# Optimization experiments

Hardware: AMD Instinct MI355X
Metric: run time of the kernel (lower is better)

Reference implementation:

```python
import jax, jax.numpy as jnp
import numpy as np

N, E, D_IN, D, H = 50000, 600000, 128, 128, 128
NEG_SLOPE = 0.2  # PyG GATConv default


def setup_inputs() -> dict:
    key = jax.random.key(0)
    ks = jax.random.split(key, 10)
    s = 1.0 / np.sqrt(D)
    return {
        "x": jax.random.normal(ks[0], (N, D_IN), jnp.float32),
        "edge_index": jax.random.randint(ks[1], (2, E), 0, N, jnp.int64),
        "h": jax.random.normal(ks[2], (1, N, H), jnp.float32),
        "c": jax.random.normal(ks[3], (1, N, H), jnp.float32),
        "W": jax.random.normal(ks[4], (D_IN, D), jnp.float32) * s,
        "att_src": jax.random.normal(ks[5], (D,), jnp.float32) * s,
        "att_dst": jax.random.normal(ks[6], (D,), jnp.float32) * s,
        "bias_gat": jnp.zeros((D,), jnp.float32),
        "W_ih": jax.random.normal(ks[7], (4 * H, D), jnp.float32) * s,
        "W_hh": jax.random.normal(ks[8], (4 * H, H), jnp.float32) * s,
    }


def _gat_conv(x, edge_index, W, att_src, att_dst, bias_gat):
    n = x.shape[0]
    xs = x @ W  # [N, D]
    # add self loops (PyG default add_self_loops=True)
    loop = jnp.arange(n, dtype=edge_index.dtype)
    src = jnp.concatenate([edge_index[0], loop])
    dst = jnp.concatenate([edge_index[1], loop])
    a_src = xs @ att_src  # [N]
    a_dst = xs @ att_dst  # [N]
    e = a_src[src] + a_dst[dst]  # [E+N]
    e = jnp.where(e >= 0, e, NEG_SLOPE * e)  # leaky_relu
    # segment softmax over edges grouped by destination node
    e_max = jax.ops.segment_max(e, dst, num_segments=n)
    e_exp = jnp.exp(e - e_max[dst])
    e_sum = jax.ops.segment_sum(e_exp, dst, num_segments=n)
    alpha = e_exp / (e_sum[dst] + 1e-16)  # [E+N]
    out = jax.ops.segment_sum(alpha[:, None] * xs[src], dst, num_segments=n)
    return out + bias_gat


def _lstm_step(x, h0, c0, W_ih, W_hh):
    # torch LSTM gate order: i, f, g, o; bias=False
    gates = x @ W_ih.T + h0 @ W_hh.T  # [N, 4H]
    i, f, g, o = jnp.split(gates, 4, axis=-1)
    i, f, o = jax.nn.sigmoid(i), jax.nn.sigmoid(f), jax.nn.sigmoid(o)
    g = jnp.tanh(g)
    c1 = f * c0 + i * g
    h1 = o * jnp.tanh(c1)
    return h1, c1


def reference(x, edge_index, h, c, W, att_src, att_dst, bias_gat, W_ih, W_hh):
    xb = jnp.tanh(_gat_conv(x, edge_index, W, att_src, att_dst, bias_gat))  # [N, D]
    h1, c1 = _lstm_step(xb, h[0], c[0], W_ih, W_hh)
    # LSTM output for seq_len=1 equals the new hidden state
    return xb * 0 + h1, h1[None], c1[None]
```

## Files before the change

kernel.cpp:

```cpp
#include <hip/hip_runtime.h>
#include <hip/hip_bf16.h>
#include <math.h>

#define NEG 0.2f

typedef float f32x4 __attribute__((ext_vector_type(4)));
typedef short bf16x8 __attribute__((ext_vector_type(8)));

__device__ __forceinline__ float fsig(float x){ return 1.0f/(1.0f+__expf(-x)); }
__device__ __forceinline__ float ftanh(float x){ float e = __expf(2.0f*x); return 1.0f - 2.0f/(e+1.0f); }
__device__ __forceinline__ unsigned short f2bf(float v){
    __hip_bfloat16 b = __float2bfloat16(v);
    return *(unsigned short*)&b;
}
__device__ __forceinline__ bf16x8 pack8(float4 u, float4 v){
    bf16x8 r;
    r[0]=(short)f2bf(u.x); r[1]=(short)f2bf(u.y); r[2]=(short)f2bf(u.z); r[3]=(short)f2bf(u.w);
    r[4]=(short)f2bf(v.x); r[5]=(short)f2bf(v.y); r[6]=(short)f2bf(v.z); r[7]=(short)f2bf(v.w);
    return r;
}

__global__ void k_probe(const int* __restrict__ ei, int* __restrict__ flag){
    if(threadIdx.x==0){
        int nz=0;
        for(int i=0;i<64;i++) nz |= ei[2*i+1];
        *flag = (nz==0) ? 1 : 0;
    }
}

__global__ __launch_bounds__(256) void k_wpackx(const float* __restrict__ W,
                                                unsigned short* __restrict__ WPX){
    int f = blockIdx.x*256 + threadIdx.x;
    int l = f&63, ct = (f>>6)&7, ks = f>>9;
    int k0 = ks*32 + (l>>4)*8;
    int col = ct*16 + (l&15);
    #pragma unroll
    for(int j=0;j<8;j++) WPX[(size_t)f*8+j] = f2bf(W[(size_t)(k0+j)*128 + col]);
}

__global__ __launch_bounds__(256) void k_wtpack2(const float* __restrict__ W_ih,
                                                 const float* __restrict__ W_hh,
                                                 unsigned short* __restrict__ WP2){
    int f = blockIdx.x*256 + threadIdx.x;
    int l = f&63, ct = (f>>6)&3, ks = (f>>8)&7, g = f>>11;
    int k0 = ks*32 + (l>>4)*8;
    int col = ct*128 + g*16 + (l&15);
    #pragma unroll
    for(int j=0;j<8;j++){
        int k = k0+j;
        float w = (k<128) ? W_ih[(size_t)col*128+k] : W_hh[(size_t)col*128+(k-128)];
        WP2[(size_t)f*8+j] = f2bf(w);
    }
}

__global__ __launch_bounds__(256,2) void k_gemm_xs3(const float* __restrict__ x,
                                                    const unsigned short* __restrict__ WPX,
                                                    const float* __restrict__ att_s,
                                                    const float* __restrict__ att_d,
                                                    unsigned short* __restrict__ xsb,
                                                    float* __restrict__ a_src,
                                                    float* __restrict__ a_dst,
                                                    int n, int ntiles, int nwaves){
    const int w = threadIdx.x>>6, l = threadIdx.x&63;
    const int wid = blockIdx.x*4 + w;
    bf16x8 B[32];
    #pragma unroll
    for(int f=0;f<32;f++) B[f] = *(const bf16x8*)(WPX + (size_t)(f*64 + l)*8);
    float asv[8], adv[8];
    #pragma unroll
    for(int ct=0;ct<8;ct++){
        asv[ct] = att_s[ct*16 + (l&15)];
        adv[ct] = att_d[ct*16 + (l&15)];
    }
    for(int rt = wid; rt < ntiles; rt += nwaves){
        int arow = rt*16 + (l&15); if(arow>=n) arow = n-1;
        const float* xr = x + (size_t)arow*128 + (l>>4)*8;
        bf16x8 A[4];
        #pragma unroll
        for(int ks=0;ks<4;ks++){
            float4 u = *(const float4*)(xr + ks*32);
            float4 v = *(const float4*)(xr + ks*32 + 4);
            A[ks] = pack8(u,v);
        }
        f32x4 acc[8];
        #pragma unroll
        for(int ct=0;ct<8;ct++) acc[ct] = (f32x4){0.f,0.f,0.f,0.f};
        #pragma unroll
        for(int ks=0;ks<4;ks++){
            #pragma unroll
            for(int ct=0;ct<8;ct++)
                acc[ct] = __builtin_amdgcn_mfma_f32_16x16x32_bf16(A[ks], B[ks*8+ct], acc[ct], 0,0,0);
        }
        #pragma unroll
        for(int reg=0;reg<4;reg++){
            int row = rt*16 + (l>>4)*4 + reg;
            float ps=0.f, pd=0.f;
            #pragma unroll
            for(int ct=0;ct<8;ct++){ ps += acc[ct][reg]*asv[ct]; pd += acc[ct][reg]*adv[ct]; }
            ps += __shfl_xor(ps,1); pd += __shfl_xor(pd,1);
            ps += __shfl_xor(ps,2); pd += __shfl_xor(pd,2);
            ps += __shfl_xor(ps,4); pd += __shfl_xor(pd,4);
            ps += __shfl_xor(ps,8); pd += __shfl_xor(pd,8);
            if((l&15)==0 && row<n){ a_src[row]=ps; a_dst[row]=pd; }
            if(row<n){
                #pragma unroll
                for(int ct=0;ct<8;ct++)
                    xsb[(size_t)row*128 + ct*16 + (l&15)] = f2bf(acc[ct][reg]);
            }
        }
    }
}

__global__ __launch_bounds__(256) void k_hist(const int* __restrict__ ei,
                                              const int* __restrict__ flag,
                                              int* __restrict__ deg, int E, int EN){
    int e = blockIdx.x*256 + threadIdx.x;
    if(e>=EN) return;
    int dst = (e>=E) ? (e-E) : (*flag ? ei[2*(E+e)] : ei[E+e]);
    atomicAdd(&deg[dst], 1);
}

__global__ __launch_bounds__(256) void k_scan1(const int* __restrict__ deg,
                                               int* __restrict__ bsum, int n){
    __shared__ int ws[4];
    int b = blockIdx.x, t = threadIdx.x;
    int i = b*512 + t*2;
    int s = 0;
    if(i<n)   s += deg[i];
    if(i+1<n) s += deg[i+1];
    for(int off=32;off;off>>=1) s += __shfl_xor(s,off);
    if((t&63)==0) ws[t>>6]=s;
    __syncthreads();
    if(t==0) bsum[b]=ws[0]+ws[1]+ws[2]+ws[3];
}

__global__ void k_scan2(int* __restrict__ bsum, int* __restrict__ rowptr,
                        int nb, int n, int EN){
    int t = threadIdx.x;
    int v0 = (t<nb)    ? bsum[t]    : 0;
    int v1 = (64+t<nb) ? bsum[64+t] : 0;
    int x = v0;
    for(int d=1; d<64; d<<=1){ int y=__shfl_up(x,d); if(t>=d) x+=y; }
    int tot0 = __shfl(x,63);
    int x1 = v1;
    for(int d=1; d<64; d<<=1){ int y=__shfl_up(x1,d); if(t>=d) x1+=y; }
    if(t<nb)    bsum[t]    = x - v0;
    if(64+t<nb) bsum[64+t] = tot0 + x1 - v1;
    if(t==0) rowptr[n]=EN;
}

__global__ __launch_bounds__(256) void k_scan3(const int* __restrict__ deg,
                                               const int* __restrict__ bsum,
                                               int* __restrict__ rowptr,
                                               int* __restrict__ cursor, int n){
    __shared__ int wsum[4];
    int b = blockIdx.x, t = threadIdx.x;
    int i = b*512 + t*2;
    int d0 = (i<n)?deg[i]:0, d1 = (i+1<n)?deg[i+1]:0;
    int s = d0+d1;
    int x = s;
    int lane = t&63, wv = t>>6;
    for(int dd=1; dd<64; dd<<=1){ int y=__shfl_up(x,dd); if(lane>=dd) x+=y; }
    if(lane==63) wsum[wv]=x;
    __syncthreads();
    int woff=0;
    for(int w=0;w<wv;w++) woff += wsum[w];
    int ex = bsum[b] + woff + x - s;
    if(i<n)   { rowptr[i]  =ex;    cursor[i]  =ex;    }
    if(i+1<n) { rowptr[i+1]=ex+d0; cursor[i+1]=ex+d0; }
}

__global__ __launch_bounds__(256) void k_fill(const int* __restrict__ ei,
                                              const int* __restrict__ flag,
                                              int* __restrict__ cursor,
                                              int* __restrict__ csr_src, int E, int EN){
    int e = blockIdx.x*256 + threadIdx.x;
    if(e>=EN) return;
    int src,dst;
    if(e>=E){ src=dst=e-E; }
    else if(*flag){ src = ei[2*e]; dst = ei[2*(E+e)]; }
    else         { src = ei[e];   dst = ei[E+e]; }
    int pos = atomicAdd(&cursor[dst], 1);
    csr_src[pos] = src;
}

__global__ __launch_bounds__(256) void k_agg3(const int* __restrict__ rowptr,
                                              const int* __restrict__ csr_src,
                                              const float* __restrict__ a_src,
                                              const float* __restrict__ a_dst,
                                              const unsigned int* __restrict__ xsb32,
                                              const float* __restrict__ bg,
                                              const float* __restrict__ h0,
                                              unsigned short* __restrict__ xh, int n){
    const int wv = threadIdx.x>>6, l = threadIdx.x&63;
    const int dst = blockIdx.x*4 + wv;
    if(dst>=n) return;
    const int beg = rowptr[dst], end = rowptr[dst+1];
    const float ad = a_dst[dst];
    float ax=0.f, ay=0.f, psum=0.f;
    int j = beg;
    for(; j+4<=end; j+=4){
        int s0=csr_src[j], s1=csr_src[j+1], s2=csr_src[j+2], s3=csr_src[j+3];
        float e0=a_src[s0]+ad, e1=a_src[s1]+ad, e2=a_src[s2]+ad, e3=a_src[s3]+ad;
        unsigned k0=xsb32[(size_t)s0*64+l], k1=xsb32[(size_t)s1*64+l];
        unsigned k2=xsb32[(size_t)s2*64+l], k3=xsb32[(size_t)s3*64+l];
        e0 = e0>=0.f?e0:NEG*e0; e1 = e1>=0.f?e1:NEG*e1;
        e2 = e2>=0.f?e2:NEG*e2; e3 = e3>=0.f?e3:NEG*e3;
        float p0=__expf(e0), p1=__expf(e1), p2=__expf(e2), p3=__expf(e3);
        psum += p0+p1+p2+p3;
        ax += p0*__uint_as_float(k0<<16) + p1*__uint_as_float(k1<<16)
            + p2*__uint_as_float(k2<<16) + p3*__uint_as_float(k3<<16);
        ay += p0*__uint_as_float(k0&0xffff0000u) + p1*__uint_as_float(k1&0xffff0000u)
            + p2*__uint_as_float(k2&0xffff0000u) + p3*__uint_as_float(k3&0xffff0000u);
    }
    for(; j<end; ++j){
        int s = csr_src[j];
        float sv = a_src[s]+ad;
        sv = sv>=0.f ? sv : NEG*sv;
        float p = __expf(sv);
        psum += p;
        unsigned pk = xsb32[(size_t)s*64 + l];
        ax += p*__uint_as_float(pk<<16);
        ay += p*__uint_as_float(pk & 0xffff0000u);
    }
    const float inv = 1.0f/(psum + 1e-16f);
    float t0 = ftanh(ax*inv + bg[2*l]);
    float t1 = ftanh(ay*inv + bg[2*l+1]);
    unsigned int pk = (unsigned)f2bf(t0) | ((unsigned)f2bf(t1)<<16);
    unsigned int* xr = (unsigned int*)(xh + (size_t)dst*256);
    xr[l] = pk;
    float2 hv = *(const float2*)(h0 + (size_t)dst*128 + 2*l);
    xr[64 + l] = (unsigned)f2bf(hv.x) | ((unsigned)f2bf(hv.y)<<16);
}

__global__ __launch_bounds__(256,2) void k_lstm5(const unsigned short* __restrict__ xh,
                                                 const unsigned short* __restrict__ WP2,
                                                 const float* __restrict__ c0,
                                                 float* __restrict__ out,
                                                 int n, int ntiles, int wstride){
    const int w = threadIdx.x>>6, l = threadIdx.x&63;
    const int wid = blockIdx.x*4 + w;
    const int g = wid & 7, wgi = wid >> 3;
    const unsigned short* wp = WP2 + (size_t)g*16384;
    bf16x8 B[32];
    #pragma unroll
    for(int f=0;f<32;f++) B[f] = *(const bf16x8*)(wp + (size_t)(f*64 + l)*8);
    const size_t nn = (size_t)n*128;
    const int col = g*16 + (l&15);
    for(int rt = wgi; rt < ntiles; rt += wstride){
        int arow = rt*16 + (l&15); if(arow>=n) arow = n-1;
        const unsigned short* ar = xh + (size_t)arow*256 + (l>>4)*8;
        bf16x8 A[8];
        #pragma unroll
        for(int ks=0;ks<8;ks++) A[ks] = *(const bf16x8*)(ar + ks*32);
        f32x4 acc[4];
        #pragma unroll
        for(int ct=0;ct<4;ct++) acc[ct] = (f32x4){0.f,0.f,0.f,0.f};
        #pragma unroll
        for(int ks=0;ks<8;ks++){
            #pragma unroll
            for(int ct=0;ct<4;ct++)
                acc[ct] = __builtin_amdgcn_mfma_f32_16x16x32_bf16(A[ks], B[ks*4+ct], acc[ct], 0,0,0);
        }
        #pragma unroll
        for(int reg=0;reg<4;reg++){
            int row = rt*16 + (l>>4)*4 + reg;
            if(row>=n) continue;
            float gi = acc[0][reg], gf = acc[1][reg];
            float gg = acc[2][reg], go = acc[3][reg];
            float cc = c0[(size_t)row*128+col];
            float c1v = fsig(gf)*cc + fsig(gi)*ftanh(gg);
            float h1v = fsig(go)*ftanh(c1v);
            out[(size_t)row*128+col]        = h1v;
            out[nn + (size_t)row*128+col]   = h1v;
            out[2*nn + (size_t)row*128+col] = c1v;
        }
    }
}

extern "C" void kernel_launch(void* const* d_in, const int* in_sizes, int n_in,
                              void* d_out, int out_size, void* d_ws, size_t ws_size,
                              hipStream_t stream) {
    const float* x      = (const float*)d_in[0];
    const int*   ei     = (const int*)  d_in[1];
    const float* h      = (const float*)d_in[2];
    const float* c      = (const float*)d_in[3];
    const float* W      = (const float*)d_in[4];
    const float* atts   = (const float*)d_in[5];
    const float* attd   = (const float*)d_in[6];
    const float* bias   = (const float*)d_in[7];
    const float* W_ih   = (const float*)d_in[8];
    const float* W_hh   = (const float*)d_in[9];
    float* out = (float*)d_out;

    const int n  = in_sizes[0]/128;
    const int E  = in_sizes[1]/2;
    const int EN = E + n;
    const int NB = (n + 511)/512;
    const int ntiles = (n + 15)/16;
    const int n2 = ntiles*16;

    unsigned short* xsb = (unsigned short*)d_ws;
    unsigned short* xh  = xsb + (size_t)n*128;
    unsigned short* WP2 = xh + (size_t)n2*256;
    unsigned short* WPX = WP2 + 131072;
    float* a_src = (float*)(WPX + 16384);
    float* a_dst = a_src + n;
    int*   deg    = (int*)(a_dst + n);
    int*   rowptr = deg + n;
    int*   cursor = rowptr + n + 1;
    int*   bsum   = cursor + n;
    int*   csr_src= bsum + 128;
    int*   flag   = csr_src + EN;

    hipMemsetAsync(deg, 0, (size_t)n*sizeof(int), stream);
    k_probe<<<1,64,0,stream>>>(ei, flag);
    k_wpackx<<<8,256,0,stream>>>(W, WPX);
    k_wtpack2<<<64,256,0,stream>>>(W_ih, W_hh, WP2);
    k_gemm_xs3<<<1024,256,0,stream>>>(x, WPX, atts, attd, xsb, a_src, a_dst, n, ntiles, 4096);
    k_hist<<<(EN+255)/256,256,0,stream>>>(ei,flag,deg,E,EN);
    k_scan1<<<NB,256,0,stream>>>(deg,bsum,n);
    k_scan2<<<1,64,0,stream>>>(bsum,rowptr,NB,n,EN);
    k_scan3<<<NB,256,0,stream>>>(deg,bsum,rowptr,cursor,n);
    k_fill<<<(EN+255)/256,256,0,stream>>>(ei,flag,cursor,csr_src,E,EN);
    k_agg3<<<(n+3)/4,256,0,stream>>>(rowptr,csr_src,a_src,a_dst,(const unsigned int*)xsb,bias,h,xh,n);
    k_lstm5<<<1024,256,0,stream>>>(xh, WP2, c, out, n, ntiles, 512);
}
```

Measured before the change: 178.9 us.

## Stage packed weights in LDS and software-prefetch next LSTM tile

Both MFMA GEMM kernels now copy their packed bf16 weight fragments into 32KB of shared memory once per block and read B operands from LDS, instead of holding 32 bf16x8 registers per lane. This frees VGPRs so launch bounds can rise to 4 blocks per SM. The LSTM kernel also double-buffers the next tile's A rows and c0 values in registers so global loads overlap the current tile's MFMAs. The grid and stride arguments change to match the new block-to-tile mapping. The cost is extra LDS traffic per MFMA and possible LDS bank conflicts.

After: 315.3 us. +76.2%, slower.

```diff
diff --git a/kernel.cpp b/kernel.cpp
--- a/kernel.cpp
+++ b/kernel.cpp
@@ -53,26 +53,31 @@
     }
 }
 
-__global__ __launch_bounds__(256,2) void k_gemm_xs3(const float* __restrict__ x,
+__global__ __launch_bounds__(256,4) void k_gemm_xs4(const float* __restrict__ x,
                                                     const unsigned short* __restrict__ WPX,
                                                     const float* __restrict__ att_s,
                                                     const float* __restrict__ att_d,
                                                     unsigned short* __restrict__ xsb,
                                                     float* __restrict__ a_src,
                                                     float* __restrict__ a_dst,
-                                                    int n, int ntiles, int nwaves){
-    const int w = threadIdx.x>>6, l = threadIdx.x&63;
-    const int wid = blockIdx.x*4 + w;
-    bf16x8 B[32];
-    #pragma unroll
-    for(int f=0;f<32;f++) B[f] = *(const bf16x8*)(WPX + (size_t)(f*64 + l)*8);
+                                                    int n, int ntiles, int nblk){
+    __shared__ unsigned short Bl[16384];
+    const int t = threadIdx.x;
+    const int w = t>>6, l = t&63;
+    {
+        const float4* gsrc = (const float4*)WPX;
+        float4* ldst = (float4*)Bl;
+        #pragma unroll
+        for(int i=0;i<8;i++) ldst[t + i*256] = gsrc[t + i*256];
+    }
+    __syncthreads();
     float asv[8], adv[8];
     #pragma unroll
     for(int ct=0;ct<8;ct++){
         asv[ct] = att_s[ct*16 + (l&15)];
         adv[ct] = att_d[ct*16 + (l&15)];
     }
-    for(int rt = wid; rt < ntiles; rt += nwaves){
+    for(int rt = blockIdx.x*4 + w; rt < ntiles; rt += nblk*4){
         int arow = rt*16 + (l&15); if(arow>=n) arow = n-1;
         const float* xr = x + (size_t)arow*128 + (l>>4)*8;
         bf16x8 A[4];
@@ -88,8 +93,10 @@
         #pragma unroll
         for(int ks=0;ks<4;ks++){
             #pragma unroll
-            for(int ct=0;ct<8;ct++)
-                acc[ct] = __builtin_amdgcn_mfma_f32_16x16x32_bf16(A[ks], B[ks*8+ct], acc[ct], 0,0,0);
+            for(int ct=0;ct<8;ct++){
+                const bf16x8 b = *(const bf16x8*)(Bl + ((ks*8+ct)*64 + l)*8);
+                acc[ct] = __builtin_amdgcn_mfma_f32_16x16x32_bf16(A[ks], b, acc[ct], 0,0,0);
+            }
         }
         #pragma unroll
         for(int reg=0;reg<4;reg++){
@@ -233,47 +240,77 @@
     xr[64 + l] = (unsigned)f2bf(hv.x) | ((unsigned)f2bf(hv.y)<<16);
 }
 
-__global__ __launch_bounds__(256,2) void k_lstm5(const unsigned short* __restrict__ xh,
+__global__ __launch_bounds__(256,4) void k_lstm6(const unsigned short* __restrict__ xh,
                                                  const unsigned short* __restrict__ WP2,
                                                  const float* __restrict__ c0,
                                                  float* __restrict__ out,
-                                                 int n, int ntiles, int wstride){
-    const int w = threadIdx.x>>6, l = threadIdx.x&63;
-    const int wid = blockIdx.x*4 + w;
-    const int g = wid & 7, wgi = wid >> 3;
-    const unsigned short* wp = WP2 + (size_t)g*16384;
-    bf16x8 B[32];
-    #pragma unroll
-    for(int f=0;f<32;f++) B[f] = *(const bf16x8*)(wp + (size_t)(f*64 + l)*8);
+                                                 int n, int ntiles, int nblk){
+    __shared__ unsigned short Bl[16384];
+    const int t = threadIdx.x;
+    const int w = t>>6, l = t&63;
+    const int g = blockIdx.x & 7;
+    {
+        const float4* gsrc = (const float4*)(WP2 + (size_t)g*16384);
+        float4* ldst = (float4*)Bl;
+        #pragma unroll
+        for(int i=0;i<8;i++) ldst[t + i*256] = gsrc[t + i*256];
+    }
+    __syncthreads();
     const size_t nn = (size_t)n*128;
     const int col = g*16 + (l&15);
-    for(int rt = wgi; rt < ntiles; rt += wstride){
-        int arow = rt*16 + (l&15); if(arow>=n) arow = n-1;
+    const int wstride = nblk*4;
+    int rt = (blockIdx.x>>3)*4 + w;
+    if(rt >= ntiles) return;
+    bf16x8 A[8]; float cc[4];
+    {
+        int arow = rt*16 + (l&15); if(arow>=n) arow=n-1;
         const unsigned short* ar = xh + (size_t)arow*256 + (l>>4)*8;
-        bf16x8 A[8];
         #pragma unroll
         for(int ks=0;ks<8;ks++) A[ks] = *(const bf16x8*)(ar + ks*32);
+        int rbase = rt*16 + (l>>4)*4;
+        #pragma unroll
+        for(int r=0;r<4;r++){ int rr=rbase+r; if(rr>=n) rr=n-1; cc[r]=c0[(size_t)rr*128+col]; }
+    }
+    while(rt < ntiles){
+        const int rtn = rt + wstride;
+        bf16x8 A2[8]; float cc2[4];
+        if(rtn < ntiles){
+            int arow = rtn*16 + (l&15); if(arow>=n) arow=n-1;
+            const unsigned short* ar = xh + (size_t)arow*256 + (l>>4)*8;
+            #pragma unroll
+            for(int ks=0;ks<8;ks++) A2[ks] = *(const bf16x8*)(ar + ks*32);
+            int rbase = rtn*16 + (l>>4)*4;
+            #pragma unroll
+            for(int r=0;r<4;r++){ int rr=rbase+r; if(rr>=n) rr=n-1; cc2[r]=c0[(size_t)rr*128+col]; }
+        }
         f32x4 acc[4];
         #pragma unroll
         for(int ct=0;ct<4;ct++) acc[ct] = (f32x4){0.f,0.f,0.f,0.f};
         #pragma unroll
         for(int ks=0;ks<8;ks++){
             #pragma unroll
-            for(int ct=0;ct<4;ct++)
-                acc[ct] = __builtin_amdgcn_mfma_f32_16x16x32_bf16(A[ks], B[ks*4+ct], acc[ct], 0,0,0);
+            for(int ct=0;ct<4;ct++){
+                const bf16x8 b = *(const bf16x8*)(Bl + ((ks*4+ct)*64 + l)*8);
+                acc[ct] = __builtin_amdgcn_mfma_f32_16x16x32_bf16(A[ks], b, acc[ct], 0,0,0);
+            }
         }
         #pragma unroll
         for(int reg=0;reg<4;reg++){
             int row = rt*16 + (l>>4)*4 + reg;
             if(row>=n) continue;
-            float gi = acc[0][reg], gf = acc[1][reg];
-            float gg = acc[2][reg], go = acc[3][reg];
-            float cc = c0[(size_t)row*128+col];
-            float c1v = fsig(gf)*cc + fsig(gi)*ftanh(gg);
+            float gi=acc[0][reg], gf=acc[1][reg], gg=acc[2][reg], go=acc[3][reg];
+            float c1v = fsig(gf)*cc[reg] + fsig(gi)*ftanh(gg);
             float h1v = fsig(go)*ftanh(c1v);
             out[(size_t)row*128+col]        = h1v;
             out[nn + (size_t)row*128+col]   = h1v;
             out[2*nn + (size_t)row*128+col] = c1v;
+        }
+        rt = rtn;
+        if(rt < ntiles){
+            #pragma unroll
+            for(int ks=0;ks<8;ks++) A[ks] = A2[ks];
+            #pragma unroll
+            for(int r=0;r<4;r++) cc[r] = cc2[r];
         }
     }
 }
@@ -317,12 +354,12 @@
     k_probe<<<1,64,0,stream>>>(ei, flag);
     k_wpackx<<<8,256,0,stream>>>(W, WPX);
     k_wtpack2<<<64,256,0,stream>>>(W_ih, W_hh, WP2);
-    k_gemm_xs3<<<1024,256,0,stream>>>(x, WPX, atts, attd, xsb, a_src, a_dst, n, ntiles, 4096);
+    k_gemm_xs4<<<512,256,0,stream>>>(x, WPX, atts, attd, xsb, a_src, a_dst, n, ntiles, 512);
     k_hist<<<(EN+255)/256,256,0,stream>>>(ei,flag,deg,E,EN);
     k_scan1<<<NB,256,0,stream>>>(deg,bsum,n);
     k_scan2<<<1,64,0,stream>>>(bsum,rowptr,NB,n,EN);
     k_scan3<<<NB,256,0,stream>>>(deg,bsum,rowptr,cursor,n);
     k_fill<<<(EN+255)/256,256,0,stream>>>(ei,flag,cursor,csr_src,E,EN);
     k_agg3<<<(n+3)/4,256,0,stream>>>(rowptr,csr_src,a_src,a_dst,(const unsigned int*)xsb,bias,h,xh,n);
-    k_lstm5<<<1024,256,0,stream>>>(xh, WP2, c, out, n, ntiles, 512);
-}
+    k_lstm6<<<1024,256,0,stream>>>(xh, WP2, c, out, n, ntiles, 128);
+}
```
